# Kernel tuning notes

Hardware: AMD Instinct MI355X
Metric: run time of the kernel (lower is better)

Reference implementation:

```python
import jax, jax.numpy as jnp
import numpy as np

N = 50000
D = 128
E = 600000
R = 8


def setup_inputs() -> dict:
    key = jax.random.key(0)
    ks = jax.random.split(key, 8)
    x = jax.random.normal(ks[0], (N, D), dtype=jnp.float32)
    edge_index = jax.random.randint(ks[1], (2, E), 0, N, dtype=jnp.int64)
    edge_type = jax.random.randint(ks[2], (E,), 0, R, dtype=jnp.int64)
    scale = 1.0 / np.sqrt(D)
    w1 = jax.random.normal(ks[3], (R, D, D), dtype=jnp.float32) * scale
    root1 = jax.random.normal(ks[4], (D, D), dtype=jnp.float32) * scale
    b1 = jnp.zeros((D,), dtype=jnp.float32)
    w2 = jax.random.normal(ks[5], (R, D, D), dtype=jnp.float32) * scale
    root2 = jax.random.normal(ks[6], (D, D), dtype=jnp.float32) * scale
    b2 = jnp.zeros((D,), dtype=jnp.float32)
    return {"x": x, "edge_index": edge_index, "edge_type": edge_type,
            "w1": w1, "root1": root1, "b1": b1,
            "w2": w2, "root2": root2, "b2": b2}


def _rgcn_conv(x, edge_index, edge_type, w, root, b):
    # PyG RGCNConv: per-relation MEAN aggregation of source features over
    # incoming edges, then relation-specific linear, summed over relations,
    # plus root transform and bias.
    src, dst = edge_index[0], edge_index[1]
    # combined segment id: (dst_node, relation) -> one segment_sum pass
    seg = dst * R + edge_type  # [E]
    msgs = x[src]              # [E, D] gather
    sums = jax.ops.segment_sum(msgs, seg, num_segments=N * R).reshape(N, R, D)
    cnts = jax.ops.segment_sum(jnp.ones((msgs.shape[0],), dtype=x.dtype), seg,
                               num_segments=N * R).reshape(N, R, 1)
    mean = sums / jnp.maximum(cnts, 1.0)  # [N, R, D]; empty -> 0
    out = jnp.einsum('nrd,rde->ne', mean, w) + x @ root + b
    return out


def reference(x, edge_index, edge_type, w1, root1, b1, w2, root2, b2):
    # dropout is identity in eval mode
    h = jax.nn.relu(_rgcn_conv(x, edge_index, edge_type, w1, root1, b1))
    out = jax.nn.relu(_rgcn_conv(h, edge_index, edge_type, w2, root2, b2))
    return out
```

## Files before the change

### kernel.cpp

```cpp
#include <hip/hip_runtime.h>

#define NN 50000
#define D 128
#define EE 600000
#define R 8
#define NR (NN * R)
#define SCAN_CHUNK 1024
#define NSB ((NR + SCAN_CHUNK - 1) / SCAN_CHUNK)
#define KO 1152

typedef unsigned short u16;
typedef unsigned int u32;
typedef __attribute__((ext_vector_type(8))) short bf16x8;
typedef __attribute__((ext_vector_type(4))) float f32x4;

__device__ inline u16 f2bf(float f) {
    union { float f; u32 u; } v; v.f = f;
    return (u16)((v.u + 0x7FFFu + ((v.u >> 16) & 1u)) >> 16);
}
__device__ inline float bf2f(u16 h) {
    union { u32 u; float f; } v; v.u = ((u32)h) << 16;
    return v.f;
}

__global__ __launch_bounds__(256) void hist_kernel(const int* __restrict__ dst,
                                                   const int* __restrict__ et,
                                                   int* __restrict__ cnt, int E) {
    int e = blockIdx.x * 256 + threadIdx.x;
    if (e < E) atomicAdd(&cnt[dst[e] * R + et[e]], 1);
}

__global__ __launch_bounds__(256) void scanA(const int* __restrict__ cnt,
                                             int* __restrict__ off,
                                             int* __restrict__ bsum) {
    __shared__ int ts[256];
    const int b = blockIdx.x, t = threadIdx.x;
    const int base = b * SCAN_CHUNK + t * 4;
    int v0 = 0, v1 = 0, v2 = 0, v3 = 0;
    if (base + 3 < NR) {
        int4 q = *(const int4*)(cnt + base);
        v0 = q.x; v1 = q.y; v2 = q.z; v3 = q.w;
    } else {
        if (base < NR) v0 = cnt[base];
        if (base + 1 < NR) v1 = cnt[base + 1];
        if (base + 2 < NR) v2 = cnt[base + 2];
    }
    const int s = v0 + v1 + v2 + v3;
    ts[t] = s;
    __syncthreads();
    for (int d = 1; d < 256; d <<= 1) {
        int x = (t >= d) ? ts[t - d] : 0;
        __syncthreads();
        ts[t] += x;
        __syncthreads();
    }
    const int excl = ts[t] - s;
    if (base < NR) off[base] = excl;
    if (base + 1 < NR) off[base + 1] = excl + v0;
    if (base + 2 < NR) off[base + 2] = excl + v0 + v1;
    if (base + 3 < NR) off[base + 3] = excl + v0 + v1 + v2;
    if (t == 255) bsum[b] = ts[255];
}

__global__ __launch_bounds__(256) void scanBC(int* __restrict__ off,
                                              int* __restrict__ cursor,
                                              const int* __restrict__ bsum) {
    __shared__ int red[256];
    const int b = blockIdx.x, t = threadIdx.x;
    int p = 0;
    for (int i = t; i < b; i += 256) p += bsum[i];
    red[t] = p;
    __syncthreads();
    for (int d = 128; d > 0; d >>= 1) {
        if (t < d) red[t] += red[t + d];
        __syncthreads();
    }
    const int add = red[0];
    const int base = b * SCAN_CHUNK + t * 4;
#pragma unroll
    for (int j = 0; j < 4; ++j)
        if (base + j < NR) {
            int v = off[base + j] + add;
            off[base + j] = v;
            cursor[base + j] = v;
        }
    if (b == 0 && t == 0) off[NR] = EE;
}

__global__ __launch_bounds__(256) void place_kernel(const int* __restrict__ src,
                                                    const int* __restrict__ dst,
                                                    const int* __restrict__ et,
                                                    int* __restrict__ cursor,
                                                    u32* __restrict__ epk, int E) {
    int e = blockIdx.x * 256 + threadIdx.x;
    if (e < E) {
        int r = et[e];
        int key = dst[e] * R + r;
        int p = atomicAdd(&cursor[key], 1);
        epk[p] = ((u32)src[e] << 3) | (u32)r;
    }
}

__global__ __launch_bounds__(256) void bprep2_kernel(const float* __restrict__ w1,
                                                     const float* __restrict__ root1,
                                                     u16* __restrict__ Bf1,
                                                     const float* __restrict__ w2,
                                                     const float* __restrict__ root2,
                                                     u16* __restrict__ Bf2,
                                                     int4* __restrict__ cntz) {
    int gidx = blockIdx.x * 256 + threadIdx.x;
    for (int i = gidx; i < NR / 4; i += 36864)
        cntz[i] = make_int4(0, 0, 0, 0);
    if (gidx >= 2 * 9 * 4 * 8 * 64) return;
    const int layer = gidx / (9 * 4 * 8 * 64);
    const int idx = gidx - layer * (9 * 4 * 8 * 64);
    const float* w = layer ? w2 : w1;
    const float* root = layer ? root2 : root1;
    u16* Bfrag = layer ? Bf2 : Bf1;
    const int lane = idx & 63;
    const int g = (idx >> 6) & 7;
    const int kc = (idx >> 9) & 3;
    const int ct = idx >> 11;
    const int col = ct * 128 + g * 16 + (lane & 15);
    const int kbase = kc * 32 + (lane >> 4) * 8;
    u16* o = Bfrag + (size_t)idx * 8;
#pragma unroll
    for (int j = 0; j < 8; ++j) {
        const int k = kbase + j;
        float v = (col < R * D) ? w[(size_t)(col >> 7) * (D * D) + (size_t)k * D + (col & 127)]
                                : root[(size_t)k * D + (col - R * D)];
        o[j] = f2bf(v);
    }
}

template <bool INF32>
__global__ __launch_bounds__(256, 4) void gemm_xw(const void* __restrict__ xin,
                                                  const u16* __restrict__ Bfrag,
                                                  u16* __restrict__ y) {
    __shared__ uint4 Bs[2048];

    const int t = threadIdx.x;
    const int wave = t >> 6;
    const int lane = t & 63;
    const int quad = lane >> 4;
    const int l15 = lane & 15;
    const int n0 = blockIdx.x * 64;
    const int n = n0 + wave * 16 + l15;
    const int nc = (n < NN) ? n : (NN - 1);

    bf16x8 a0, a1, a2, a3;
    if (INF32) {
        const float* xr = (const float*)xin + (size_t)nc * D + quad * 8;
#pragma unroll
        for (int c = 0; c < 4; ++c) {
            float4 v0 = *(const float4*)(xr + c * 32);
            float4 v1 = *(const float4*)(xr + c * 32 + 4);
            bf16x8 a;
            a[0] = (short)f2bf(v0.x); a[1] = (short)f2bf(v0.y);
            a[2] = (short)f2bf(v0.z); a[3] = (short)f2bf(v0.w);
            a[4] = (short)f2bf(v1.x); a[5] = (short)f2bf(v1.y);
            a[6] = (short)f2bf(v1.z); a[7] = (short)f2bf(v1.w);
            if (c == 0) a0 = a; else if (c == 1) a1 = a;
            else if (c == 2) a2 = a; else a3 = a;
        }
    } else {
        const u16* xr = (const u16*)xin + (size_t)nc * D + quad * 8;
        a0 = *(const bf16x8*)(xr);
        a1 = *(const bf16x8*)(xr + 32);
        a2 = *(const bf16x8*)(xr + 64);
        a3 = *(const bf16x8*)(xr + 96);
    }

#pragma unroll 1
    for (int ct = 0; ct < 9; ++ct) {
        const uint4* bsrc = (const uint4*)Bfrag + (size_t)ct * 2048 + t;

        __syncthreads();
#pragma unroll
        for (int i = 0; i < 8; ++i) Bs[t + 256 * i] = bsrc[256 * i];
        __syncthreads();

        f32x4 acc[8];
#pragma unroll
        for (int g = 0; g < 8; ++g) acc[g] = (f32x4){0.f, 0.f, 0.f, 0.f};

        const u16* bb = (const u16*)Bs + lane * 8;
#pragma unroll
        for (int g = 0; g < 8; ++g) {
            bf16x8 b0 = *(const bf16x8*)(bb + (0 * 8 + g) * 512);
            acc[g] = __builtin_amdgcn_mfma_f32_16x16x32_bf16(a0, b0, acc[g], 0, 0, 0);
            bf16x8 b1 = *(const bf16x8*)(bb + (1 * 8 + g) * 512);
            acc[g] = __builtin_amdgcn_mfma_f32_16x16x32_bf16(a1, b1, acc[g], 0, 0, 0);
            bf16x8 b2 = *(const bf16x8*)(bb + (2 * 8 + g) * 512);
            acc[g] = __builtin_amdgcn_mfma_f32_16x16x32_bf16(a2, b2, acc[g], 0, 0, 0);
            bf16x8 b3 = *(const bf16x8*)(bb + (3 * 8 + g) * 512);
            acc[g] = __builtin_amdgcn_mfma_f32_16x16x32_bf16(a3, b3, acc[g], 0, 0, 0);
        }

#pragma unroll
        for (int g = 0; g < 8; ++g) {
            const int col = ct * 128 + g * 16 + l15;
#pragma unroll
            for (int q = 0; q < 4; ++q) {
                const int row = n0 + wave * 16 + quad * 4 + q;
                if (row < NN)
                    y[(size_t)row * KO + col] = f2bf(acc[g][q]);
            }
        }
    }
}

template <bool OUTBF>
__global__ __launch_bounds__(256) void agg_kernel(const u32* __restrict__ yv,
                                                  const int* __restrict__ off,
                                                  const u32* __restrict__ epk,
                                                  const int* __restrict__ cnt,
                                                  const float* __restrict__ bias,
                                                  void* __restrict__ outp) {
    const int n = blockIdx.x * 4 + (threadIdx.x >> 6);
    const int lane = threadIdx.x & 63;
    const int e0 = off[n * 8], e1 = off[n * 8 + 8];

    float ax = 0.f, ay = 0.f;
    int cbase = e0;
    u32 yoff = 0u; float sc = 0.f;
    if (cbase + lane < e1) {
        const u32 pk = epk[cbase + lane];
        const int r = (int)(pk & 7u);
        yoff = (pk >> 3) * (KO / 2) + (u32)r * (D / 2);
        sc = 1.0f / (float)cnt[n * 8 + r];
    }

    int i = e0;
    while (i < e1) {
        const int chunk_end = (e1 < cbase + 64) ? e1 : (cbase + 64);
        for (; i + 3 < chunk_end; i += 4) {
            const int j = i - cbase;
            const u32 p0 = (u32)__shfl((int)yoff, j);
            const u32 p1 = (u32)__shfl((int)yoff, j + 1);
            const u32 p2 = (u32)__shfl((int)yoff, j + 2);
            const u32 p3 = (u32)__shfl((int)yoff, j + 3);
            const float f0 = __shfl(sc, j);
            const float f1 = __shfl(sc, j + 1);
            const float f2 = __shfl(sc, j + 2);
            const float f3 = __shfl(sc, j + 3);
            const u32 v0 = yv[(size_t)p0 + lane];
            const u32 v1 = yv[(size_t)p1 + lane];
            const u32 v2 = yv[(size_t)p2 + lane];
            const u32 v3 = yv[(size_t)p3 + lane];
            ax += f0 * bf2f((u16)(v0 & 0xFFFFu)); ay += f0 * bf2f((u16)(v0 >> 16));
            ax += f1 * bf2f((u16)(v1 & 0xFFFFu)); ay += f1 * bf2f((u16)(v1 >> 16));
            ax += f2 * bf2f((u16)(v2 & 0xFFFFu)); ay += f2 * bf2f((u16)(v2 >> 16));
            ax += f3 * bf2f((u16)(v3 & 0xFFFFu)); ay += f3 * bf2f((u16)(v3 >> 16));
        }
        for (; i < chunk_end; ++i) {
            const int j = i - cbase;
            const u32 p0 = (u32)__shfl((int)yoff, j);
            const float f0 = __shfl(sc, j);
            const u32 v0 = yv[(size_t)p0 + lane];
            ax += f0 * bf2f((u16)(v0 & 0xFFFFu));
            ay += f0 * bf2f((u16)(v0 >> 16));
        }
        if (i < e1) {
            cbase += 64;
            if (cbase + lane < e1) {
                const u32 pk = epk[cbase + lane];
                const int r = (int)(pk & 7u);
                yoff = (pk >> 3) * (KO / 2) + (u32)r * (D / 2);
                sc = 1.0f / (float)cnt[n * 8 + r];
            } else { yoff = 0u; sc = 0.f; }
        }
    }

    const u32 rv = yv[(size_t)n * (KO / 2) + (R * D / 2) + lane];
    const float2 bb = ((const float2*)bias)[lane];
    const float ox = fmaxf(ax + bf2f((u16)(rv & 0xFFFFu)) + bb.x, 0.f);
    const float oy = fmaxf(ay + bf2f((u16)(rv >> 16)) + bb.y, 0.f);
    if (OUTBF)
        ((u32*)outp)[(size_t)n * 64 + lane] = (u32)f2bf(ox) | ((u32)f2bf(oy) << 16);
    else
        ((float2*)outp)[(size_t)n * 64 + lane] = make_float2(ox, oy);
}

extern "C" void kernel_launch(void* const* d_in, const int* in_sizes, int n_in,
                              void* d_out, int out_size, void* d_ws, size_t ws_size,
                              hipStream_t stream) {
    const float* x = (const float*)d_in[0];
    const int* ei = (const int*)d_in[1];
    const int* et = (const int*)d_in[2];
    const float* w1 = (const float*)d_in[3];
    const float* root1 = (const float*)d_in[4];
    const float* b1 = (const float*)d_in[5];
    const float* w2 = (const float*)d_in[6];
    const float* root2 = (const float*)d_in[7];
    const float* b2 = (const float*)d_in[8];
    float* out = (float*)d_out;

    char* ws = (char*)d_ws;
    int* off    = (int*)(ws + 0);
    int* cnt_i  = (int*)(ws + 1600512);
    int* cursor = (int*)(ws + 3200512);
    int* bsum   = (int*)(ws + 4800512);
    u32* epk    = (u32*)(ws + 4804096);
    u32* h      = (u32*)(ws + 7204096);
    u16* y      = (u16*)(ws + 20004096);
    u16* Bf1    = (u16*)(ws + 135204096);
    u16* Bf2    = (u16*)(ws + 135499008);

    const int* srcp = ei;
    const int* dstp = ei + EE;

    bprep2_kernel<<<144, 256, 0, stream>>>(w1, root1, Bf1, w2, root2, Bf2,
                                           (int4*)cnt_i);
    hist_kernel<<<(EE + 255) / 256, 256, 0, stream>>>(dstp, et, cnt_i, EE);
    scanA<<<NSB, 256, 0, stream>>>(cnt_i, off, bsum);
    scanBC<<<NSB, 256, 0, stream>>>(off, cursor, bsum);
    place_kernel<<<(EE + 255) / 256, 256, 0, stream>>>(srcp, dstp, et, cursor,
                                                       epk, EE);

    const int gemm_blocks = (NN + 63) / 64;
    const int agg_blocks = NN / 4;

    gemm_xw<true><<<gemm_blocks, 256, 0, stream>>>(x, Bf1, y);
    agg_kernel<true><<<agg_blocks, 256, 0, stream>>>((const u32*)y, off, epk,
                                                     cnt_i, b1, h);

    gemm_xw<false><<<gemm_blocks, 256, 0, stream>>>(h, Bf2, y);
    agg_kernel<false><<<agg_blocks, 256, 0, stream>>>((const u32*)y, off, epk,
                                                      cnt_i, b2, out);
}
```

Measured before the change: 284.7 us.

## Fuse aggregation and GEMM: aggregate-then-transform per node tile with K=1152 MFMA

Reorders each RGCN layer from transform-then-aggregate (a GEMM that writes a 1152-wide Y buffer, then a gather over Y) to aggregate-then-transform. Each block gathers per-relation mean features of 128-wide bf16 inputs into a swizzled LDS A tile, then runs a K=1152 MFMA against the stacked relation and root weights. This removes the large intermediate Y write and re-read and shrinks the gathered rows from the Y layout to the narrower bf16 input rows. A separate cast kernel converts x to bf16 first. The trade-offs are a serial per-relation gather loop in each wave and B fragments read directly from global memory without LDS staging.

```diff
diff --git a/kernel.cpp b/kernel.cpp
--- a/kernel.cpp
+++ b/kernel.cpp
@@ -7,7 +7,7 @@
 #define NR (NN * R)
 #define SCAN_CHUNK 1024
 #define NSB ((NR + SCAN_CHUNK - 1) / SCAN_CHUNK)
-#define KO 1152
+#define KT 36
 
 typedef unsigned short u16;
 typedef unsigned int u32;
@@ -111,175 +111,129 @@
     int gidx = blockIdx.x * 256 + threadIdx.x;
     for (int i = gidx; i < NR / 4; i += 36864)
         cntz[i] = make_int4(0, 0, 0, 0);
-    if (gidx >= 2 * 9 * 4 * 8 * 64) return;
-    const int layer = gidx / (9 * 4 * 8 * 64);
-    const int idx = gidx - layer * (9 * 4 * 8 * 64);
+    if (gidx >= 2 * KT * 8 * 64) return;
+    const int layer = gidx / (KT * 8 * 64);
+    const int idx = gidx - layer * (KT * 8 * 64);
     const float* w = layer ? w2 : w1;
     const float* root = layer ? root2 : root1;
     u16* Bfrag = layer ? Bf2 : Bf1;
     const int lane = idx & 63;
     const int g = (idx >> 6) & 7;
-    const int kc = (idx >> 9) & 3;
-    const int ct = idx >> 11;
-    const int col = ct * 128 + g * 16 + (lane & 15);
-    const int kbase = kc * 32 + (lane >> 4) * 8;
+    const int kt = idx >> 9;
+    const int col = g * 16 + (lane & 15);
+    const int kbase = kt * 32 + (lane >> 4) * 8;
     u16* o = Bfrag + (size_t)idx * 8;
 #pragma unroll
     for (int j = 0; j < 8; ++j) {
         const int k = kbase + j;
-        float v = (col < R * D) ? w[(size_t)(col >> 7) * (D * D) + (size_t)k * D + (col & 127)]
-                                : root[(size_t)k * D + (col - R * D)];
+        float v = (k < R * D) ? w[(size_t)(k >> 7) * (D * D) + (size_t)(k & 127) * D + col]
+                              : root[(size_t)(k - R * D) * D + col];
         o[j] = f2bf(v);
     }
 }
 
-template <bool INF32>
-__global__ __launch_bounds__(256, 4) void gemm_xw(const void* __restrict__ xin,
-                                                  const u16* __restrict__ Bfrag,
-                                                  u16* __restrict__ y) {
-    __shared__ uint4 Bs[2048];
+__global__ __launch_bounds__(256) void xcast_kernel(const float4* __restrict__ x,
+                                                    u32* __restrict__ xb) {
+    int i = blockIdx.x * 256 + threadIdx.x;
+    if (i < NN * 32) {
+        float4 v = x[i];
+        xb[i * 2] = (u32)f2bf(v.x) | ((u32)f2bf(v.y) << 16);
+        xb[i * 2 + 1] = (u32)f2bf(v.z) | ((u32)f2bf(v.w) << 16);
+    }
+}
+
+template <bool OUTBF>
+__global__ __launch_bounds__(512, 4) void rgcn_fused(const u32* __restrict__ xb,
+                                                     const u16* __restrict__ Bf,
+                                                     const int* __restrict__ off,
+                                                     const u32* __restrict__ epk,
+                                                     const float* __restrict__ bias,
+                                                     void* __restrict__ outp) {
+    __shared__ u32 A32[KT * 2 * 256];
 
     const int t = threadIdx.x;
-    const int wave = t >> 6;
+    const int wid = t >> 6;
     const int lane = t & 63;
+    const int n0 = blockIdx.x * 32;
+
+    const int q2 = (lane & 15) >> 2;
+    const int ktl = lane >> 4;
+    const int xv = q2 | ((ktl & 1) << 2);
+
+#pragma unroll 1
+    for (int ii = 0; ii < 4; ++ii) {
+        const int i = wid * 4 + ii;
+        const int n = n0 + i;
+        const int nc = (n < NN) ? n : (NN - 1);
+        int offv = 0;
+        if (lane < 9) offv = off[nc * 8 + lane];
+        const int e0 = __shfl(offv, 0);
+        const int e1 = __shfl(offv, 8);
+        u32 epkv = 0u;
+        if (e0 + lane < e1) epkv = epk[e0 + lane];
+
+        const int mt = i >> 4;
+        const int lrow = i & 15;
+        const int wbase = (((lrow ^ xv) + 16 * q2) << 2) + (lane & 3);
+
+#pragma unroll 1
+        for (int r = 0; r < 8; ++r) {
+            const int se = __shfl(offv, r);
+            const int ee = __shfl(offv, r + 1);
+            float sx = 0.f, sy = 0.f;
+            for (int p = se; p < ee; ++p) {
+                const int j = p - e0;
+                u32 pk;
+                if (j < 64) pk = (u32)__shfl((int)epkv, j);
+                else pk = epk[p];
+                const u32 v = xb[(size_t)(pk >> 3) * 64 + lane];
+                sx += bf2f((u16)(v & 0xFFFFu));
+                sy += bf2f((u16)(v >> 16));
+            }
+            const float inv = (ee > se) ? 1.f / (float)(ee - se) : 0.f;
+            const int kt = r * 4 + ktl;
+            A32[(kt * 2 + mt) * 256 + wbase] =
+                (u32)f2bf(sx * inv) | ((u32)f2bf(sy * inv) << 16);
+        }
+        A32[((32 + ktl) * 2 + mt) * 256 + wbase] = xb[(size_t)nc * 64 + lane];
+    }
+    __syncthreads();
+
+    const int g = wid;
+    f32x4 accL = {0.f, 0.f, 0.f, 0.f}, accH = {0.f, 0.f, 0.f, 0.f};
+    const u16* bp = Bf + ((size_t)g * 64 + lane) * 8;
+    const u16* A16 = (const u16*)A32;
+#pragma unroll 4
+    for (int kt = 0; kt < KT; ++kt) {
+        const bf16x8 b = *(const bf16x8*)(bp + (size_t)kt * 4096);
+        const int xvr = (lane >> 4) | ((kt & 1) << 2);
+        const int lp = (lane ^ xvr) * 8;
+        const bf16x8 a0 = *(const bf16x8*)(A16 + (kt * 2 + 0) * 512 + lp);
+        const bf16x8 a1 = *(const bf16x8*)(A16 + (kt * 2 + 1) * 512 + lp);
+        accL = __builtin_amdgcn_mfma_f32_16x16x32_bf16(a0, b, accL, 0, 0, 0);
+        accH = __builtin_amdgcn_mfma_f32_16x16x32_bf16(a1, b, accH, 0, 0, 0);
+    }
+
     const int quad = lane >> 4;
     const int l15 = lane & 15;
-    const int n0 = blockIdx.x * 64;
-    const int n = n0 + wave * 16 + l15;
-    const int nc = (n < NN) ? n : (NN - 1);
-
-    bf16x8 a0, a1, a2, a3;
-    if (INF32) {
-        const float* xr = (const float*)xin + (size_t)nc * D + quad * 8;
+    const int col = g * 16 + l15;
+    const float bb = bias[col];
 #pragma unroll
-        for (int c = 0; c < 4; ++c) {
-            float4 v0 = *(const float4*)(xr + c * 32);
-            float4 v1 = *(const float4*)(xr + c * 32 + 4);
-            bf16x8 a;
-            a[0] = (short)f2bf(v0.x); a[1] = (short)f2bf(v0.y);
-            a[2] = (short)f2bf(v0.z); a[3] = (short)f2bf(v0.w);
-            a[4] = (short)f2bf(v1.x); a[5] = (short)f2bf(v1.y);
-            a[6] = (short)f2bf(v1.z); a[7] = (short)f2bf(v1.w);
-            if (c == 0) a0 = a; else if (c == 1) a1 = a;
-            else if (c == 2) a2 = a; else a3 = a;
+    for (int q = 0; q < 4; ++q) {
+        const int rL = n0 + quad * 4 + q;
+        const int rH = rL + 16;
+        const float vL = fmaxf(accL[q] + bb, 0.f);
+        const float vH = fmaxf(accH[q] + bb, 0.f);
+        if (OUTBF) {
+            u16* hp = (u16*)outp;
+            if (rL < NN) hp[(size_t)rL * D + col] = f2bf(vL);
+            if (rH < NN) hp[(size_t)rH * D + col] = f2bf(vH);
+        } else {
+            float* op = (float*)outp;
+            if (rL < NN) op[(size_t)rL * D + col] = vL;
+            if (rH < NN) op[(size_t)rH * D + col] = vH;
         }
-    } else {
-        const u16* xr = (const u16*)xin + (size_t)nc * D + quad * 8;
-        a0 = *(const bf16x8*)(xr);
-        a1 = *(const bf16x8*)(xr + 32);
-        a2 = *(const bf16x8*)(xr + 64);
-        a3 = *(const bf16x8*)(xr + 96);
-    }
-
-#pragma unroll 1
-    for (int ct = 0; ct < 9; ++ct) {
-        const uint4* bsrc = (const uint4*)Bfrag + (size_t)ct * 2048 + t;
-
-        __syncthreads();
-#pragma unroll
-        for (int i = 0; i < 8; ++i) Bs[t + 256 * i] = bsrc[256 * i];
-        __syncthreads();
-
-        f32x4 acc[8];
-#pragma unroll
-        for (int g = 0; g < 8; ++g) acc[g] = (f32x4){0.f, 0.f, 0.f, 0.f};
-
-        const u16* bb = (const u16*)Bs + lane * 8;
-#pragma unroll
-        for (int g = 0; g < 8; ++g) {
-            bf16x8 b0 = *(const bf16x8*)(bb + (0 * 8 + g) * 512);
-            acc[g] = __builtin_amdgcn_mfma_f32_16x16x32_bf16(a0, b0, acc[g], 0, 0, 0);
-            bf16x8 b1 = *(const bf16x8*)(bb + (1 * 8 + g) * 512);
-            acc[g] = __builtin_amdgcn_mfma_f32_16x16x32_bf16(a1, b1, acc[g], 0, 0, 0);
-            bf16x8 b2 = *(const bf16x8*)(bb + (2 * 8 + g) * 512);
-            acc[g] = __builtin_amdgcn_mfma_f32_16x16x32_bf16(a2, b2, acc[g], 0, 0, 0);
-            bf16x8 b3 = *(const bf16x8*)(bb + (3 * 8 + g) * 512);
-            acc[g] = __builtin_amdgcn_mfma_f32_16x16x32_bf16(a3, b3, acc[g], 0, 0, 0);
-        }
-
-#pragma unroll
-        for (int g = 0; g < 8; ++g) {
-            const int col = ct * 128 + g * 16 + l15;
-#pragma unroll
-            for (int q = 0; q < 4; ++q) {
-                const int row = n0 + wave * 16 + quad * 4 + q;
-                if (row < NN)
-                    y[(size_t)row * KO + col] = f2bf(acc[g][q]);
-            }
-        }
-    }
-}
-
-template <bool OUTBF>
-__global__ __launch_bounds__(256) void agg_kernel(const u32* __restrict__ yv,
-                                                  const int* __restrict__ off,
-                                                  const u32* __restrict__ epk,
-                                                  const int* __restrict__ cnt,
-                                                  const float* __restrict__ bias,
-                                                  void* __restrict__ outp) {
-    const int n = blockIdx.x * 4 + (threadIdx.x >> 6);
-    const int lane = threadIdx.x & 63;
-    const int e0 = off[n * 8], e1 = off[n * 8 + 8];
-
-    float ax = 0.f, ay = 0.f;
-    int cbase = e0;
-    u32 yoff = 0u; float sc = 0.f;
-    if (cbase + lane < e1) {
-        const u32 pk = epk[cbase + lane];
-        const int r = (int)(pk & 7u);
-        yoff = (pk >> 3) * (KO / 2) + (u32)r * (D / 2);
-        sc = 1.0f / (float)cnt[n * 8 + r];
-    }
-
-    int i = e0;
-    while (i < e1) {
-        const int chunk_end = (e1 < cbase + 64) ? e1 : (cbase + 64);
-        for (; i + 3 < chunk_end; i += 4) {
-            const int j = i - cbase;
-            const u32 p0 = (u32)__shfl((int)yoff, j);
-            const u32 p1 = (u32)__shfl((int)yoff, j + 1);
-            const u32 p2 = (u32)__shfl((int)yoff, j + 2);
-            const u32 p3 = (u32)__shfl((int)yoff, j + 3);
-            const float f0 = __shfl(sc, j);
-            const float f1 = __shfl(sc, j + 1);
-            const float f2 = __shfl(sc, j + 2);
-            const float f3 = __shfl(sc, j + 3);
-            const u32 v0 = yv[(size_t)p0 + lane];
-            const u32 v1 = yv[(size_t)p1 + lane];
-            const u32 v2 = yv[(size_t)p2 + lane];
-            const u32 v3 = yv[(size_t)p3 + lane];
-            ax += f0 * bf2f((u16)(v0 & 0xFFFFu)); ay += f0 * bf2f((u16)(v0 >> 16));
-            ax += f1 * bf2f((u16)(v1 & 0xFFFFu)); ay += f1 * bf2f((u16)(v1 >> 16));
-            ax += f2 * bf2f((u16)(v2 & 0xFFFFu)); ay += f2 * bf2f((u16)(v2 >> 16));
-            ax += f3 * bf2f((u16)(v3 & 0xFFFFu)); ay += f3 * bf2f((u16)(v3 >> 16));
-        }
-        for (; i < chunk_end; ++i) {
-            const int j = i - cbase;
-            const u32 p0 = (u32)__shfl((int)yoff, j);
-            const float f0 = __shfl(sc, j);
-            const u32 v0 = yv[(size_t)p0 + lane];
-            ax += f0 * bf2f((u16)(v0 & 0xFFFFu));
-            ay += f0 * bf2f((u16)(v0 >> 16));
-        }
-        if (i < e1) {
-            cbase += 64;
-            if (cbase + lane < e1) {
-                const u32 pk = epk[cbase + lane];
-                const int r = (int)(pk & 7u);
-                yoff = (pk >> 3) * (KO / 2) + (u32)r * (D / 2);
-                sc = 1.0f / (float)cnt[n * 8 + r];
-            } else { yoff = 0u; sc = 0.f; }
-        }
-    }
-
-    const u32 rv = yv[(size_t)n * (KO / 2) + (R * D / 2) + lane];
-    const float2 bb = ((const float2*)bias)[lane];
-    const float ox = fmaxf(ax + bf2f((u16)(rv & 0xFFFFu)) + bb.x, 0.f);
-    const float oy = fmaxf(ay + bf2f((u16)(rv >> 16)) + bb.y, 0.f);
-    if (OUTBF)
-        ((u32*)outp)[(size_t)n * 64 + lane] = (u32)f2bf(ox) | ((u32)f2bf(oy) << 16);
-    else
-        ((float2*)outp)[(size_t)n * 64 + lane] = make_float2(ox, oy);
+    }
 }
 
 extern "C" void kernel_launch(void* const* d_in, const int* in_sizes, int n_in,
@@ -302,30 +256,27 @@
     int* cursor = (int*)(ws + 3200512);
     int* bsum   = (int*)(ws + 4800512);
     u32* epk    = (u32*)(ws + 4804096);
-    u32* h      = (u32*)(ws + 7204096);
-    u16* y      = (u16*)(ws + 20004096);
-    u16* Bf1    = (u16*)(ws + 135204096);
-    u16* Bf2    = (u16*)(ws + 135499008);
+    u32* xb     = (u32*)(ws + 7204096);
+    u32* h      = (u32*)(ws + 20004096);
+    u16* Bf1    = (u16*)(ws + 32804096);
+    u16* Bf2    = (u16*)(ws + 33099008);
 
     const int* srcp = ei;
     const int* dstp = ei + EE;
 
     bprep2_kernel<<<144, 256, 0, stream>>>(w1, root1, Bf1, w2, root2, Bf2,
                                            (int4*)cnt_i);
+    xcast_kernel<<<(NN * 32 + 255) / 256, 256, 0, stream>>>((const float4*)x, xb);
     hist_kernel<<<(EE + 255) / 256, 256, 0, stream>>>(dstp, et, cnt_i, EE);
     scanA<<<NSB, 256, 0, stream>>>(cnt_i, off, bsum);
     scanBC<<<NSB, 256, 0, stream>>>(off, cursor, bsum);
     place_kernel<<<(EE + 255) / 256, 256, 0, stream>>>(srcp, dstp, et, cursor,
                                                        epk, EE);
 
-    const int gemm_blocks = (NN + 63) / 64;
-    const int agg_blocks = NN / 4;
-
-    gemm_xw<true><<<gemm_blocks, 256, 0, stream>>>(x, Bf1, y);
-    agg_kernel<true><<<agg_blocks, 256, 0, stream>>>((const u32*)y, off, epk,
-                                                     cnt_i, b1, h);
-
-    gemm_xw<false><<<gemm_blocks, 256, 0, stream>>>(h, Bf2, y);
-    agg_kernel<false><<<agg_blocks, 256, 0, stream>>>((const u32*)y, off, epk,
-                                                      cnt_i, b2, out);
-}
+    const int fused_blocks = (NN + 31) / 32;
+
+    rgcn_fused<true><<<fused_blocks, 512, 0, stream>>>(xb, Bf1, off, epk, b1,
+                                                       (void*)h);
+    rgcn_fused<false><<<fused_blocks, 512, 0, stream>>>(h, Bf2, off, epk, b2,
+                                                        (void*)out);
+}
```

New measurement: 410.1 us. 1.44x slower.
